# Performance work log

Hardware: AMD Instinct MI355X
Metric: run time of the kernel (lower is better)

Reference implementation:

```python
import jax, jax.numpy as jnp
import numpy as np

B, L, D, DI, DS, DC, DTR = 128, 31, 1024, 2048, 16, 5, 64

def setup_inputs() -> dict:
    key = jax.random.key(0)
    ks = jax.random.split(key, 12)
    rn = lambda k, shp, s=0.02: jax.random.normal(k, shp, dtype=jnp.float32) * s
    return {
        "x": jax.random.normal(ks[0], (B, L, D), dtype=jnp.float32),
        "norm1_w": jnp.ones((D,), jnp.float32), "norm1_b": jnp.zeros((D,), jnp.float32),
        "in_proj_W": rn(ks[1], (2 * DI, D)),
        "conv_w": rn(ks[2], (DI, DC), 0.2), "conv_b": jnp.zeros((DI,), jnp.float32),
        "x_proj_W": rn(ks[3], (DTR + 2 * DS, DI)),
        "dt_proj_W": rn(ks[4], (DI, DTR), 0.1),
        "dt_proj_b": jnp.full((DI,), -4.6, dtype=jnp.float32),  # softplus^-1(~0.01)
        "A_log": jnp.tile(jnp.log(jnp.arange(1, DS + 1, dtype=jnp.float32))[None, :], (DI, 1)),
        "D_ssm": jnp.ones((DI,), jnp.float32),
        "out_proj_W": rn(ks[5], (D, DI)),
        "norm2_w": jnp.ones((D,), jnp.float32), "norm2_b": jnp.zeros((D,), jnp.float32),
        "ffn_W1": rn(ks[6], (2 * D, D)), "ffn_b1": jnp.zeros((2 * D,), jnp.float32),
        "ffn_W2": rn(ks[7], (D, 2 * D)), "ffn_b2": jnp.zeros((D,), jnp.float32),
        "cls_W1": rn(ks[8], (D, L * D)), "cls_b1": jnp.zeros((D,), jnp.float32),
        "cls_W2": rn(ks[9], (1, D)), "cls_b2": jnp.zeros((1,), jnp.float32),
    }

def _ln(x, w, b):
    m = x.mean(-1, keepdims=True)
    v = x.var(-1, keepdims=True)
    return (x - m) * jax.lax.rsqrt(v + 1e-5) * w + b

def _mamba(x, in_proj_W, conv_w, conv_b, x_proj_W, dt_proj_W, dt_proj_b, A_log, D_ssm, out_proj_W):
    # in_proj -> (u, z)
    xz = jnp.einsum('bld,ed->ble', x, in_proj_W)            # (B,L,2*DI)
    u, z = jnp.split(xz, 2, axis=-1)
    # causal depthwise conv1d (kernel DC) + SiLU
    xp = jnp.pad(u, ((0, 0), (DC - 1, 0), (0, 0)))
    uc = conv_b + sum(xp[:, k:k + L, :] * conv_w[:, k] for k in range(DC))
    uc = jax.nn.silu(uc)
    # input-dependent dt, B, C
    x_dbl = jnp.einsum('bld,ed->ble', uc, x_proj_W)         # (B,L,DTR+2*DS)
    dt, Bm, Cm = jnp.split(x_dbl, [DTR, DTR + DS], axis=-1)
    dt = jax.nn.softplus(jnp.einsum('blr,dr->bld', dt, dt_proj_W) + dt_proj_b)
    A = -jnp.exp(A_log)                                      # (DI,DS)
    def step(h, ins):
        dt_t, B_t, C_t, u_t = ins                            # (B,DI),(B,DS),(B,DS),(B,DI)
        dA = jnp.exp(dt_t[:, :, None] * A)                   # (B,DI,DS)
        h = h * dA + dt_t[:, :, None] * B_t[:, None, :] * u_t[:, :, None]
        y = jnp.einsum('bds,bs->bd', h, C_t)
        return h, y
    h0 = jnp.zeros((u.shape[0], DI, DS), u.dtype)
    _, ys = jax.lax.scan(step, h0, (dt.transpose(1, 0, 2), Bm.transpose(1, 0, 2),
                                    Cm.transpose(1, 0, 2), uc.transpose(1, 0, 2)))
    y = ys.transpose(1, 0, 2) + uc * D_ssm                   # skip term D*u
    y = y * jax.nn.silu(z)                                   # gate
    return jnp.einsum('bld,ed->ble', y, out_proj_W)

def reference(x, norm1_w, norm1_b, in_proj_W, conv_w, conv_b, x_proj_W, dt_proj_W,
              dt_proj_b, A_log, D_ssm, out_proj_W, norm2_w, norm2_b, ffn_W1, ffn_b1,
              ffn_W2, ffn_b2, cls_W1, cls_b1, cls_W2, cls_b2):
    # single encoder block (n_layers=1), dropout = identity (eval)
    res = x
    h = _ln(x, norm1_w, norm1_b)
    h = _mamba(h, in_proj_W, conv_w, conv_b, x_proj_W, dt_proj_W, dt_proj_b,
               A_log, D_ssm, out_proj_W)
    x = res + h
    res = x
    h = _ln(x, norm2_w, norm2_b)
    h = jax.nn.silu(jnp.einsum('bld,ed->ble', h, ffn_W1) + ffn_b1)
    h = jnp.einsum('ble,de->bld', h, ffn_W2) + ffn_b2
    x = res + h
    # classifier: Flatten -> Linear -> SiLU -> Linear
    flat = x.reshape(x.shape[0], -1)                          # (B, L*D)
    c = jax.nn.silu(flat @ cls_W1.T + cls_b1)
    out = c @ cls_W2.T + cls_b2                               # (B,1)
    return (out, x)
```

## Files before the change

kernel.cpp:

```cpp
#include <hip/hip_runtime.h>
#include <cstddef>
#include <cstdint>

#define B_   128
#define L_   31
#define D_   1024
#define DI_  2048
#define DS_  16
#define DC_  5
#define DTR_ 64
#define ROWS (B_ * L_)
#define KCLS (L_ * D_)

#define W_IN  0
#define W_OUT 4194304
#define W_F1  6291456
#define W_F2  8388608
#define W_XP  10485760
#define W_DT  10747904
#define WTOT  10878976

typedef unsigned short u16;
typedef __attribute__((ext_vector_type(8))) short s16x8;
typedef __attribute__((ext_vector_type(4))) float f32x4;

__device__ __forceinline__ float silu_f(float x) { return x / (1.0f + __expf(-x)); }

__device__ __forceinline__ u16 f2b(float f) {
    union { float f; uint32_t u; } c; c.f = f;
    uint32_t u = c.u + 0x7FFF + ((c.u >> 16) & 1);
    return (u16)(u >> 16);
}
__device__ __forceinline__ float b2f(u16 b) {
    union { uint32_t u; float f; } c; c.u = ((uint32_t)b) << 16;
    return c.f;
}
__device__ __forceinline__ uint32_t pack2(float lo, float hi) {
    return (uint32_t)f2b(lo) | ((uint32_t)f2b(hi) << 16);
}
__device__ __forceinline__ void cvt8(const float* __restrict__ s, u16* __restrict__ d) {
    const float4* p = (const float4*)s;
    float4 a = p[0], b = p[1];
    uint4 r;
    r.x = pack2(a.x, a.y); r.y = pack2(a.z, a.w);
    r.z = pack2(b.x, b.y); r.w = pack2(b.z, b.w);
    *(uint4*)d = r;
}

#define GLD16(g, s) __builtin_amdgcn_global_load_lds( \
    (const __attribute__((address_space(1))) void*)(g), \
    (__attribute__((address_space(3))) void*)(s), 16, 0, 0)

__global__ __launch_bounds__(256) void f2b_all_kernel(
    const float* __restrict__ inW, const float* __restrict__ outW,
    const float* __restrict__ f1W, const float* __restrict__ f2W,
    const float* __restrict__ xpW, const float* __restrict__ dtW,
    u16* __restrict__ wbuf)
{
    int g = blockIdx.x * 256 + threadIdx.x;
    if (g < 524288) { cvt8(inW + (size_t)g * 8, wbuf + W_IN + (size_t)g * 8); return; }
    g -= 524288;
    if (g < 262144) { cvt8(outW + (size_t)g * 8, wbuf + W_OUT + (size_t)g * 8); return; }
    g -= 262144;
    if (g < 262144) { cvt8(f1W + (size_t)g * 8, wbuf + W_F1 + (size_t)g * 8); return; }
    g -= 262144;
    if (g < 262144) { cvt8(f2W + (size_t)g * 8, wbuf + W_F2 + (size_t)g * 8); return; }
    g -= 262144;
    if (g < 32768) {
        const int row = g >> 8, col8 = (g & 255) * 8;
        u16* d = wbuf + W_XP + (size_t)row * 2048 + col8;
        if (row < 96) cvt8(xpW + (size_t)row * 2048 + col8, d);
        else *(uint4*)d = make_uint4(0, 0, 0, 0);
        return;
    }
    g -= 32768;
    if (g < 16384) cvt8(dtW + (size_t)g * 8, wbuf + W_DT + (size_t)g * 8);
}

__global__ __launch_bounds__(256) void ln_kernel(const float* __restrict__ x,
                                                 const float* __restrict__ w,
                                                 const float* __restrict__ b,
                                                 u16* __restrict__ y)
{
    const int row = blockIdx.x;
    const float* xr = x + (size_t)row * D_;
    float v[4];
    float sum = 0.f, sq = 0.f;
#pragma unroll
    for (int i = 0; i < 4; i++) {
        v[i] = xr[threadIdx.x + i * 256];
        sum += v[i];
        sq  += v[i] * v[i];
    }
#pragma unroll
    for (int o = 32; o > 0; o >>= 1) {
        sum += __shfl_down(sum, o, 64);
        sq  += __shfl_down(sq, o, 64);
    }
    __shared__ float red[8];
    const int wid = threadIdx.x >> 6;
    if ((threadIdx.x & 63) == 0) { red[wid] = sum; red[4 + wid] = sq; }
    __syncthreads();
    sum = red[0] + red[1] + red[2] + red[3];
    sq  = red[4] + red[5] + red[6] + red[7];
    const float mean = sum * (1.0f / D_);
    const float var  = sq * (1.0f / D_) - mean * mean;
    const float rstd = rsqrtf(var + 1e-5f);
    u16* yr = y + (size_t)row * D_;
#pragma unroll
    for (int i = 0; i < 4; i++) {
        const int c = threadIdx.x + i * 256;
        yr[c] = f2b((v[i] - mean) * rstd * w[c] + b[c]);
    }
}

template <int ACT, bool BIAS, bool RES, int OUT>
__global__ __launch_bounds__(256) void gemm_mfma(
    const u16* __restrict__ A, const u16* __restrict__ W,
    const float* __restrict__ bias, const float* __restrict__ res,
    void* __restrict__ Cout, int M, int K, int Nout, int kLen)
{
    __shared__ __align__(16) u16 As[128 * 32];
    __shared__ __align__(16) u16 Bs[128 * 32];
    const int tid = threadIdx.x;
    const int l = tid & 63, w = tid >> 6;
    const int bm = blockIdx.y * 128, bn = blockIdx.x * 128;
    const int kOff = blockIdx.z * kLen;

    const int sr = l >> 2;
    const int sk = (l & 3) * 8;
    const u16* gA = A + (size_t)(bm + w * 16 + sr) * K + kOff + sk;
    const u16* gB = W + (size_t)(bn + w * 16 + sr) * K + kOff + sk;
    u16* lA = As + (w * 16 + sr) * 32 + sk;
    u16* lB = Bs + (w * 16 + sr) * 32 + sk;

    const int lane15 = l & 15, lhi = l >> 4;
    const int wr = w >> 1, wc = w & 1;
    const u16* fA = As + (wr * 64 + lane15) * 32 + lhi * 8;
    const u16* fB = Bs + (wc * 64 + lane15) * 32 + lhi * 8;

    f32x4 acc[4][4] = {};

    for (int kk = 0; kk < kLen; kk += 32) {
        GLD16(gA, lA); GLD16(gA + (size_t)64 * K, lA + 64 * 32);
        GLD16(gB, lB); GLD16(gB + (size_t)64 * K, lB + 64 * 32);
        gA += 32; gB += 32;
        __syncthreads();
        s16x8 af[4], bfr[4];
#pragma unroll
        for (int mi = 0; mi < 4; mi++) af[mi]  = *(const s16x8*)(fA + mi * 16 * 32);
#pragma unroll
        for (int ni = 0; ni < 4; ni++) bfr[ni] = *(const s16x8*)(fB + ni * 16 * 32);
#pragma unroll
        for (int mi = 0; mi < 4; mi++)
#pragma unroll
            for (int ni = 0; ni < 4; ni++)
                acc[mi][ni] = __builtin_amdgcn_mfma_f32_16x16x32_bf16(
                    af[mi], bfr[ni], acc[mi][ni], 0, 0, 0);
        __syncthreads();
    }

#pragma unroll
    for (int ni = 0; ni < 4; ni++) {
        const int col = bn + wc * 64 + ni * 16 + lane15;
        if (col >= Nout) continue;
        const float bv = BIAS ? bias[col] : 0.0f;
#pragma unroll
        for (int mi = 0; mi < 4; mi++) {
#pragma unroll
            for (int r = 0; r < 4; r++) {
                const int row = bm + wr * 64 + mi * 16 + lhi * 4 + r;
                float v = acc[mi][ni][r] + bv;
                if (ACT == 1) v = silu_f(v);
                if (ACT == 2) v = (v > 20.0f) ? v : log1pf(__expf(v));
                if (RES) v += res[(size_t)row * Nout + col];
                if (OUT == 0) ((float*)Cout)[(size_t)row * Nout + col] = v;
                if (OUT == 1) ((u16*)Cout)[(size_t)row * Nout + col] = f2b(v);
                if (OUT == 2) atomicAdd(&((float*)Cout)[(size_t)row * Nout + col], v);
            }
        }
    }
}

#define KCH 512
__global__ __launch_bounds__(256) void gemm_cls_mfma(
    const float* __restrict__ A, const float* __restrict__ W,
    float* __restrict__ C)
{
    __shared__ __align__(16) u16 As[128 * 32];
    __shared__ __align__(16) u16 Bs[128 * 32];
    const int tid = threadIdx.x;
    const int l = tid & 63, w = tid >> 6;
    const int bn = blockIdx.x * 128;
    const int k0 = blockIdx.y * KCH;

    const int sr = l >> 2;
    const int sk = (l & 3) * 8;
    const int row = w * 16 + sr;
    const float* gA0 = A + (size_t)row * KCLS + k0 + sk;
    const float* gA1 = gA0 + (size_t)64 * KCLS;
    const float* gB0 = W + (size_t)(bn + row) * KCLS + k0 + sk;
    const float* gB1 = gB0 + (size_t)64 * KCLS;
    u16* lA0 = As + row * 32 + sk;  u16* lA1 = lA0 + 64 * 32;
    u16* lB0 = Bs + row * 32 + sk;  u16* lB1 = lB0 + 64 * 32;

    const int lane15 = l & 15, lhi = l >> 4;
    const int wr = w >> 1, wc = w & 1;
    const u16* fA = As + (wr * 64 + lane15) * 32 + lhi * 8;
    const u16* fB = Bs + (wc * 64 + lane15) * 32 + lhi * 8;

    f32x4 acc[4][4] = {};

    for (int ks = 0; ks < KCH / 32; ks++) {
        float4 a00 = *(const float4*)(gA0);     float4 a01 = *(const float4*)(gA0 + 4);
        float4 a10 = *(const float4*)(gA1);     float4 a11 = *(const float4*)(gA1 + 4);
        float4 b00 = *(const float4*)(gB0);     float4 b01 = *(const float4*)(gB0 + 4);
        float4 b10 = *(const float4*)(gB1);     float4 b11 = *(const float4*)(gB1 + 4);
        gA0 += 32; gA1 += 32; gB0 += 32; gB1 += 32;
        __syncthreads();
        uint4 r;
        r.x = pack2(a00.x, a00.y); r.y = pack2(a00.z, a00.w);
        r.z = pack2(a01.x, a01.y); r.w = pack2(a01.z, a01.w);
        *(uint4*)lA0 = r;
        r.x = pack2(a10.x, a10.y); r.y = pack2(a10.z, a10.w);
        r.z = pack2(a11.x, a11.y); r.w = pack2(a11.z, a11.w);
        *(uint4*)lA1 = r;
        r.x = pack2(b00.x, b00.y); r.y = pack2(b00.z, b00.w);
        r.z = pack2(b01.x, b01.y); r.w = pack2(b01.z, b01.w);
        *(uint4*)lB0 = r;
        r.x = pack2(b10.x, b10.y); r.y = pack2(b10.z, b10.w);
        r.z = pack2(b11.x, b11.y); r.w = pack2(b11.z, b11.w);
        *(uint4*)lB1 = r;
        __syncthreads();
        s16x8 af[4], bfr[4];
#pragma unroll
        for (int mi = 0; mi < 4; mi++) af[mi]  = *(const s16x8*)(fA + mi * 16 * 32);
#pragma unroll
        for (int ni = 0; ni < 4; ni++) bfr[ni] = *(const s16x8*)(fB + ni * 16 * 32);
#pragma unroll
        for (int mi = 0; mi < 4; mi++)
#pragma unroll
            for (int ni = 0; ni < 4; ni++)
                acc[mi][ni] = __builtin_amdgcn_mfma_f32_16x16x32_bf16(
                    af[mi], bfr[ni], acc[mi][ni], 0, 0, 0);
    }

#pragma unroll
    for (int ni = 0; ni < 4; ni++) {
        const int col = bn + wc * 64 + ni * 16 + lane15;
#pragma unroll
        for (int mi = 0; mi < 4; mi++) {
#pragma unroll
            for (int r = 0; r < 4; r++) {
                const int m = wr * 64 + mi * 16 + lhi * 4 + r;
                atomicAdd(&C[(size_t)m * 1024 + col], acc[mi][ni][r]);
            }
        }
    }
}

__global__ __launch_bounds__(256) void conv_silu_kernel(const u16* __restrict__ xz,
                                                        const float* __restrict__ cw,
                                                        const float* __restrict__ cb,
                                                        u16* __restrict__ uc)
{
    const int idx = blockIdx.x * 256 + threadIdx.x;
    const int d  = idx & (DI_ - 1);
    const int bl = idx >> 11;
    const int l  = bl % L_;
    const int b  = bl / L_;
    const u16* u = xz + (size_t)b * L_ * (2 * DI_) + d;
    float acc = cb[d];
#pragma unroll
    for (int k = 0; k < DC_; k++) {
        const int ll = l + k - (DC_ - 1);
        if (ll >= 0) acc = fmaf(b2f(u[(size_t)ll * (2 * DI_)]), cw[d * DC_ + k], acc);
    }
    uc[(size_t)bl * DI_ + d] = f2b(silu_f(acc));
}

__global__ __launch_bounds__(256) void dtext_kernel(const float* __restrict__ xdbl,
                                                    u16* __restrict__ dtb)
{
    const int idx = blockIdx.x * 256 + threadIdx.x;
    const int row = idx >> 4, c4 = (idx & 15) * 4;
    float4 v = *(const float4*)(xdbl + (size_t)row * 96 + c4);
    uint2 r;
    r.x = pack2(v.x, v.y); r.y = pack2(v.z, v.w);
    *(uint2*)(dtb + (size_t)row * 64 + c4) = r;
}

__global__ __launch_bounds__(256) void scan_kernel(const u16* __restrict__ dt,
                                                   const u16* __restrict__ uc,
                                                   const u16* __restrict__ xz,
                                                   const float* __restrict__ xdbl,
                                                   const float* __restrict__ A_log,
                                                   const float* __restrict__ D_ssm,
                                                   u16* __restrict__ y)
{
    const int idx = blockIdx.x * 256 + threadIdx.x;
    const int d = idx & (DI_ - 1);
    const int b = idx >> 11;
    float A[DS_];
#pragma unroll
    for (int s = 0; s < DS_; s++) A[s] = -__expf(A_log[d * DS_ + s]);
    const float Dv = D_ssm[d];
    float h[DS_] = {};
    for (int l = 0; l < L_; l++) {
        const size_t bl = (size_t)b * L_ + l;
        const float dtv = b2f(dt[bl * DI_ + d]);
        const float uv  = b2f(uc[bl * DI_ + d]);
        const float zv  = b2f(xz[bl * (2 * DI_) + DI_ + d]);
        const float* Bp = xdbl + bl * (DTR_ + 2 * DS_) + DTR_;
        const float* Cp = Bp + DS_;
        float yv = 0.f;
#pragma unroll
        for (int s = 0; s < DS_; s++) {
            h[s] = fmaf(h[s], __expf(dtv * A[s]), dtv * Bp[s] * uv);
            yv = fmaf(h[s], Cp[s], yv);
        }
        yv = fmaf(uv, Dv, yv);
        yv *= silu_f(zv);
        y[bl * DI_ + d] = f2b(yv);
    }
}

__global__ __launch_bounds__(256) void cls2_kernel(const float* __restrict__ c,
                                                   const float* __restrict__ b1,
                                                   const float* __restrict__ W2,
                                                   const float* __restrict__ b2,
                                                   float* __restrict__ out)
{
    const int b = blockIdx.x;
    float s = 0.f;
    for (int n = threadIdx.x; n < D_; n += 256) {
        float v = c[b * D_ + n] + b1[n];
        v = silu_f(v);
        s = fmaf(v, W2[n], s);
    }
#pragma unroll
    for (int o = 32; o > 0; o >>= 1) s += __shfl_down(s, o, 64);
    __shared__ float red[4];
    const int wid = threadIdx.x >> 6;
    if ((threadIdx.x & 63) == 0) red[wid] = s;
    __syncthreads();
    if (threadIdx.x == 0) out[b] = red[0] + red[1] + red[2] + red[3] + b2[0];
}

extern "C" void kernel_launch(void* const* d_in, const int* in_sizes, int n_in,
                              void* d_out, int out_size, void* d_ws, size_t ws_size,
                              hipStream_t stream)
{
    const float* x         = (const float*)d_in[0];
    const float* n1w       = (const float*)d_in[1];
    const float* n1b       = (const float*)d_in[2];
    const float* in_projW  = (const float*)d_in[3];
    const float* conv_w    = (const float*)d_in[4];
    const float* conv_b    = (const float*)d_in[5];
    const float* x_projW   = (const float*)d_in[6];
    const float* dt_projW  = (const float*)d_in[7];
    const float* dt_projb  = (const float*)d_in[8];
    const float* A_log     = (const float*)d_in[9];
    const float* D_ssm     = (const float*)d_in[10];
    const float* out_projW = (const float*)d_in[11];
    const float* n2w       = (const float*)d_in[12];
    const float* n2b       = (const float*)d_in[13];
    const float* ffn_W1    = (const float*)d_in[14];
    const float* ffn_b1    = (const float*)d_in[15];
    const float* ffn_W2    = (const float*)d_in[16];
    const float* ffn_b2    = (const float*)d_in[17];
    const float* cls_W1    = (const float*)d_in[18];
    const float* cls_b1    = (const float*)d_in[19];
    const float* cls_W2    = (const float*)d_in[20];
    const float* cls_b2    = (const float*)d_in[21];

    float* ws   = (float*)d_ws;
    u16*   xz_b = (u16*)ws;
    u16*   uc_b = xz_b + (size_t)ROWS * 4096;
    u16*   dt_b = uc_b + (size_t)ROWS * 2048;
    u16*   y_b  = dt_b + (size_t)ROWS * 2048;
    u16*   h_b  = y_b + (size_t)ROWS * 2048;
    float* x2   = (float*)(h_b + (size_t)ROWS * 1024);
    float* xdbl = x2 + (size_t)ROWS * 1024;
    u16*   dtb  = (u16*)(xdbl + (size_t)ROWS * 96);
    u16*   wbuf = dtb + (size_t)ROWS * 64;
    float* clsh = (float*)(wbuf + (size_t)WTOT);

    float* outv = (float*)d_out;
    float* x3   = outv + B_;

    f2b_all_kernel<<<dim3(5312), dim3(256), 0, stream>>>(
        in_projW, out_projW, ffn_W1, ffn_W2, x_projW, dt_projW, wbuf);
    ln_kernel<<<dim3(ROWS), dim3(256), 0, stream>>>(x, n1w, n1b, h_b);
    gemm_mfma<0, false, false, 1><<<dim3(32, 31, 1), dim3(256), 0, stream>>>(
        h_b, wbuf + W_IN, nullptr, nullptr, xz_b, ROWS, D_, 2 * DI_, D_);
    conv_silu_kernel<<<dim3(ROWS * DI_ / 256), dim3(256), 0, stream>>>(xz_b, conv_w, conv_b, uc_b);
    hipMemsetAsync(xdbl, 0, (size_t)ROWS * 96 * sizeof(float), stream);
    gemm_mfma<0, false, false, 2><<<dim3(1, 31, 4), dim3(256), 0, stream>>>(
        uc_b, wbuf + W_XP, nullptr, nullptr, xdbl, ROWS, DI_, DTR_ + 2 * DS_, 512);
    dtext_kernel<<<dim3(ROWS * 16 / 256), dim3(256), 0, stream>>>(xdbl, dtb);
    gemm_mfma<2, true, false, 1><<<dim3(16, 31, 1), dim3(256), 0, stream>>>(
        dtb, wbuf + W_DT, dt_projb, nullptr, dt_b, ROWS, DTR_, DI_, DTR_);
    scan_kernel<<<dim3(B_ * DI_ / 256), dim3(256), 0, stream>>>(
        dt_b, uc_b, xz_b, xdbl, A_log, D_ssm, y_b);
    gemm_mfma<0, false, true, 0><<<dim3(8, 31, 1), dim3(256), 0, stream>>>(
        y_b, wbuf + W_OUT, nullptr, x, x2, ROWS, DI_, D_, DI_);
    ln_kernel<<<dim3(ROWS), dim3(256), 0, stream>>>(x2, n2w, n2b, h_b);
    gemm_mfma<1, true, false, 1><<<dim3(16, 31, 1), dim3(256), 0, stream>>>(
        h_b, wbuf + W_F1, ffn_b1, nullptr, uc_b, ROWS, D_, 2 * D_, D_);
    gemm_mfma<0, true, true, 0><<<dim3(8, 31, 1), dim3(256), 0, stream>>>(
        uc_b, wbuf + W_F2, ffn_b2, x2, x3, ROWS, 2 * D_, D_, 2 * D_);
    hipMemsetAsync(clsh, 0, (size_t)B_ * D_ * sizeof(float), stream);
    gemm_cls_mfma<<<dim3(1024 / 128, KCLS / KCH), dim3(256), 0, stream>>>(x3, cls_W1, clsh);
    cls2_kernel<<<dim3(B_), dim3(256), 0, stream>>>(clsh, cls_b1, cls_W2, cls_b2, outv);
}
```

Baseline: 437.5 us.

## Split-K the out_proj and FFN2 GEMMs with partial buffers and fused reductions

The out_proj and FFN2 GEMMs, which launched only 248 blocks, now run with a split-K of 2 and write partial sums into a scratch buffer. The partials are summed in a fused residual+LayerNorm kernel and in a new add3+bias kernel. The x_proj GEMM's atomic split-K factor goes from 4 to 16. The goal is to fill more compute units on small-grid GEMMs, at the cost of extra memory traffic for partial buffers and more atomics.

Result: faster. 425.6 us (-2.7%).

```diff
diff --git a/kernel.cpp b/kernel.cpp
--- a/kernel.cpp
+++ b/kernel.cpp
@@ -114,6 +114,68 @@
     }
 }
 
+__global__ __launch_bounds__(256) void ln2_fuse_kernel(const float* __restrict__ x,
+                                                       const float* __restrict__ p0,
+                                                       const float* __restrict__ p1,
+                                                       const float* __restrict__ w,
+                                                       const float* __restrict__ b,
+                                                       float* __restrict__ x2,
+                                                       u16* __restrict__ y)
+{
+    const int row = blockIdx.x;
+    const size_t base = (size_t)row * D_;
+    float v[4];
+    float sum = 0.f, sq = 0.f;
+#pragma unroll
+    for (int i = 0; i < 4; i++) {
+        const int c = threadIdx.x + i * 256;
+        const float s = x[base + c] + p0[base + c] + p1[base + c];
+        x2[base + c] = s;
+        v[i] = s;
+        sum += s;
+        sq  += s * s;
+    }
+#pragma unroll
+    for (int o = 32; o > 0; o >>= 1) {
+        sum += __shfl_down(sum, o, 64);
+        sq  += __shfl_down(sq, o, 64);
+    }
+    __shared__ float red[8];
+    const int wid = threadIdx.x >> 6;
+    if ((threadIdx.x & 63) == 0) { red[wid] = sum; red[4 + wid] = sq; }
+    __syncthreads();
+    sum = red[0] + red[1] + red[2] + red[3];
+    sq  = red[4] + red[5] + red[6] + red[7];
+    const float mean = sum * (1.0f / D_);
+    const float var  = sq * (1.0f / D_) - mean * mean;
+    const float rstd = rsqrtf(var + 1e-5f);
+    u16* yr = y + base;
+#pragma unroll
+    for (int i = 0; i < 4; i++) {
+        const int c = threadIdx.x + i * 256;
+        yr[c] = f2b((v[i] - mean) * rstd * w[c] + b[c]);
+    }
+}
+
+__global__ __launch_bounds__(256) void add3_bias_kernel(const float* __restrict__ x2,
+                                                        const float* __restrict__ q0,
+                                                        const float* __restrict__ q1,
+                                                        const float* __restrict__ b2,
+                                                        float* __restrict__ x3)
+{
+    const int i = blockIdx.x * 256 + threadIdx.x;
+    float4 a  = ((const float4*)x2)[i];
+    float4 c0 = ((const float4*)q0)[i];
+    float4 c1 = ((const float4*)q1)[i];
+    float4 bb = ((const float4*)b2)[i & 255];
+    float4 r;
+    r.x = a.x + c0.x + c1.x + bb.x;
+    r.y = a.y + c0.y + c1.y + bb.y;
+    r.z = a.z + c0.z + c1.z + bb.z;
+    r.w = a.w + c0.w + c1.w + bb.w;
+    ((float4*)x3)[i] = r;
+}
+
 template <int ACT, bool BIAS, bool RES, int OUT>
 __global__ __launch_bounds__(256) void gemm_mfma(
     const u16* __restrict__ A, const u16* __restrict__ W,
@@ -177,6 +239,7 @@
                 if (OUT == 0) ((float*)Cout)[(size_t)row * Nout + col] = v;
                 if (OUT == 1) ((u16*)Cout)[(size_t)row * Nout + col] = f2b(v);
                 if (OUT == 2) atomicAdd(&((float*)Cout)[(size_t)row * Nout + col], v);
+                if (OUT == 3) ((float*)Cout)[((size_t)blockIdx.z * M + row) * Nout + col] = v;
             }
         }
     }
@@ -385,6 +448,7 @@
     u16*   dtb  = (u16*)(xdbl + (size_t)ROWS * 96);
     u16*   wbuf = dtb + (size_t)ROWS * 64;
     float* clsh = (float*)(wbuf + (size_t)WTOT);
+    float* pq   = clsh + (size_t)B_ * D_;
 
     float* outv = (float*)d_out;
     float* x3   = outv + B_;
@@ -396,20 +460,23 @@
         h_b, wbuf + W_IN, nullptr, nullptr, xz_b, ROWS, D_, 2 * DI_, D_);
     conv_silu_kernel<<<dim3(ROWS * DI_ / 256), dim3(256), 0, stream>>>(xz_b, conv_w, conv_b, uc_b);
     hipMemsetAsync(xdbl, 0, (size_t)ROWS * 96 * sizeof(float), stream);
-    gemm_mfma<0, false, false, 2><<<dim3(1, 31, 4), dim3(256), 0, stream>>>(
-        uc_b, wbuf + W_XP, nullptr, nullptr, xdbl, ROWS, DI_, DTR_ + 2 * DS_, 512);
+    gemm_mfma<0, false, false, 2><<<dim3(1, 31, 16), dim3(256), 0, stream>>>(
+        uc_b, wbuf + W_XP, nullptr, nullptr, xdbl, ROWS, DI_, DTR_ + 2 * DS_, 128);
     dtext_kernel<<<dim3(ROWS * 16 / 256), dim3(256), 0, stream>>>(xdbl, dtb);
     gemm_mfma<2, true, false, 1><<<dim3(16, 31, 1), dim3(256), 0, stream>>>(
         dtb, wbuf + W_DT, dt_projb, nullptr, dt_b, ROWS, DTR_, DI_, DTR_);
     scan_kernel<<<dim3(B_ * DI_ / 256), dim3(256), 0, stream>>>(
         dt_b, uc_b, xz_b, xdbl, A_log, D_ssm, y_b);
-    gemm_mfma<0, false, true, 0><<<dim3(8, 31, 1), dim3(256), 0, stream>>>(
-        y_b, wbuf + W_OUT, nullptr, x, x2, ROWS, DI_, D_, DI_);
-    ln_kernel<<<dim3(ROWS), dim3(256), 0, stream>>>(x2, n2w, n2b, h_b);
+    gemm_mfma<0, false, false, 3><<<dim3(8, 31, 2), dim3(256), 0, stream>>>(
+        y_b, wbuf + W_OUT, nullptr, nullptr, pq, ROWS, DI_, D_, 1024);
+    ln2_fuse_kernel<<<dim3(ROWS), dim3(256), 0, stream>>>(
+        x, pq, pq + (size_t)ROWS * D_, n2w, n2b, x2, h_b);
     gemm_mfma<1, true, false, 1><<<dim3(16, 31, 1), dim3(256), 0, stream>>>(
         h_b, wbuf + W_F1, ffn_b1, nullptr, uc_b, ROWS, D_, 2 * D_, D_);
-    gemm_mfma<0, true, true, 0><<<dim3(8, 31, 1), dim3(256), 0, stream>>>(
-        uc_b, wbuf + W_F2, ffn_b2, x2, x3, ROWS, 2 * D_, D_, 2 * D_);
+    gemm_mfma<0, false, false, 3><<<dim3(8, 31, 2), dim3(256), 0, stream>>>(
+        uc_b, wbuf + W_F2, nullptr, nullptr, pq, ROWS, 2 * D_, D_, 1024);
+    add3_bias_kernel<<<dim3(ROWS * D_ / 4 / 256), dim3(256), 0, stream>>>(
+        x2, pq, pq + (size_t)ROWS * D_, ffn_b2, x3);
     hipMemsetAsync(clsh, 0, (size_t)B_ * D_ * sizeof(float), stream);
     gemm_cls_mfma<<<dim3(1024 / 128, KCLS / KCH), dim3(256), 0, stream>>>(x3, cls_W1, clsh);
     cls2_kernel<<<dim3(B_), dim3(256), 0, stream>>>(clsh, cls_b1, cls_W2, cls_b2, outv);
```
